# Optimization experiments

Measured on AMD Instinct MI355X. Metric: run time of the kernel, lower is better.

## Reference

```python
import jax, jax.numpy as jnp
import numpy as np

RESET_ALPHA = 0.9
THR_ALPHA = 0.95
DAMPENING = 0.3
REFRACTORY = 5


def setup_inputs() -> dict:
    key = jax.random.key(0)
    B, T, N = 16, 4096, 1024
    x = jax.random.normal(key, (B, T, N), dtype=jnp.float32)
    return {
        "x": x,
        "reset_gamma": jnp.ones((N,), jnp.float32),
        "thr_gamma": jnp.ones((N,), jnp.float32),
        "u0": jnp.zeros((N,), jnp.float32),
        "b0": jnp.zeros((N,), jnp.float32),
    }


def _spike(v):
    # SpikeFunction: heaviside forward, piecewise-quadratic surrogate gradient
    zf = (v > 0).astype(v.dtype)
    zb = jnp.where(v > 0, -0.5 * jnp.square(v - 1.0), 0.5 * jnp.square(v + 1.0))
    zb = jnp.where(jnp.abs(v) < 1.0, zb, 0.0) * DAMPENING
    # value == zf, gradient flows through zb (straight-through surrogate)
    return jax.lax.stop_gradient(zf - zb) + zb


def reference(x, reset_gamma, thr_gamma, u0, b0):
    B, T, N = x.shape
    al, bet = RESET_ALPHA, THR_ALPHA

    def step(carry, xt):
        u, b, q, last_z = carry  # all [B, N]
        u = al * u + (1.0 - al) * xt - last_z * reset_gamma
        z = _spike(u - b)
        z = jnp.where(q == 0, z, jnp.zeros_like(z))  # refractory mask
        q = jnp.maximum(0, q - 1)
        q = q + REFRACTORY * jax.lax.stop_gradient(z).astype(jnp.int32)
        b = bet * b + (1.0 - bet) * z * thr_gamma
        return (u, b, q, z), z

    u = jnp.broadcast_to(u0[None, :], (B, N)).astype(x.dtype)
    b = jnp.broadcast_to(b0[None, :], (B, N)).astype(x.dtype)
    q = jnp.zeros((B, N), jnp.int32)
    last_z = jnp.zeros((B, N), x.dtype)

    x_tbn = jnp.swapaxes(x, 0, 1)  # [T, B, N] for scan over time
    _, zs = jax.lax.scan(step, (u, b, q, last_z), x_tbn)
    return jnp.swapaxes(zs, 0, 1)  # [B, T, N]
```

## Files before the change

kernel.cpp:

```cpp
#include <hip/hip_runtime.h>


#pragma STDC FP_CONTRACT OFF

constexpr int B_LEN = 16;
constexpr int T_LEN = 4096;
constexpr int N_LEN = 1024;
constexpr int DEPTH = 16;
constexpr int NCH   = T_LEN / DEPTH;

__global__ __launch_bounds__(64)
void snn_fwd(const float* __restrict__ x,
             const float* __restrict__ rg_,
             const float* __restrict__ tg_,
             const float* __restrict__ u0_,
             const float* __restrict__ b0_,
             float* __restrict__ out)
{
    #pragma clang fp contract(off)
    const int id   = blockIdx.x * blockDim.x + threadIdx.x;
    const int b    = id >> 10;
    const int n    = id & 1023;
    const int loff = b * (T_LEN * N_LEN) + n;

    const float rg = rg_[n];
    const float tg = tg_[n];
    float u  = u0_[n];
    float bb = b0_[n];
    float lz = 0.0f;
    int allow = 0;

    float bufA[DEPTH], bufB[DEPTH];
    float zA[DEPTH],   zB[DEPTH];

#define LBURST(BUF, CIDX)                                                   \
    {                                                                       \
        const int cc_ = (CIDX) < NCH ? (CIDX) : (NCH - 1);                  \
        const float* p_ = x + (size_t)cc_ * (DEPTH * N_LEN) + loff;         \
        _Pragma("unroll")                                                   \
        for (int i_ = 0; i_ < DEPTH; ++i_) BUF[i_] = p_[(size_t)i_ * N_LEN];\
    }

#define SBURST(ZB_, CIDX)                                                   \
    {                                                                       \
        float* p_ = out + (size_t)(CIDX) * (DEPTH * N_LEN) + loff;          \
        _Pragma("unroll")                                                   \
        for (int i_ = 0; i_ < DEPTH; ++i_) p_[(size_t)i_ * N_LEN] = ZB_[i_];\
    }

#define COMPUTE(BUF, ZOUT, CIDX)                                            \
    {                                                                       \
        const int t0_ = (CIDX) * DEPTH;                                     \
        _Pragma("unroll")                                                   \
        for (int i_ = 0; i_ < DEPTH; ++i_) {                                \
            const float xt = BUF[i_];                                       \
            float m2 = 0.1f * xt;                                           \
            float s1 = __builtin_fmaf(0.9f, u, m2);                         \
            u = __builtin_fmaf(-lz, rg, s1);                                \
            const float v   = u - bb;                                       \
            const bool  pos = v > 0.0f;                                     \
            const float vm  = v + (pos ? -1.0f : 1.0f);                     \
            const float sq  = vm * vm;                                      \
            float zb = (pos ? -0.5f : 0.5f) * sq;                           \
            zb = (fabsf(v) < 1.0f) ? zb : 0.0f;                             \
            zb = zb * 0.3f;                                                 \
            const float zf = pos ? 1.0f : 0.0f;                             \
            const float d1 = zf - zb;                                       \
            float z = d1 + zb;                                              \
            z = ((t0_ + i_) >= allow) ? z : 0.0f;                           \
            allow = (z == 1.0f) ? (t0_ + i_ + 6) : allow;                   \
            float t1 = 0.05f * z;                                           \
            float t2 = t1 * tg;                                             \
            bb = __builtin_fmaf(0.95f, bb, t2);                             \
            lz = z;                                                         \
            ZOUT[i_] = z;                                                   \
        }                                                                   \
    }

    LBURST(bufA, 0)
    LBURST(bufB, 1)

    for (int k = 0; k < NCH; k += 2) {
        COMPUTE(bufA, zA, k)
        LBURST(bufA, k + 2)
        SBURST(zA, k)

        COMPUTE(bufB, zB, k + 1)
        LBURST(bufB, k + 3)
        SBURST(zB, k + 1)
    }
#undef LBURST
#undef SBURST
#undef COMPUTE
}

extern "C" void kernel_launch(void* const* d_in, const int* in_sizes, int n_in,
                              void* d_out, int out_size, void* d_ws, size_t ws_size,
                              hipStream_t stream)
{
    int xi = 0;
    for (int i = 1; i < n_in; ++i)
        if (in_sizes[i] > in_sizes[xi]) xi = i;

    const float* small[4];
    int k = 0;
    for (int i = 0; i < n_in && k < 4; ++i)
        if (i != xi) small[k++] = (const float*)d_in[i];

    const float* x  = (const float*)d_in[xi];
    float*      out = (float*)d_out;

    dim3 block(64);
    dim3 grid(B_LEN * N_LEN / 64);
    snn_fwd<<<grid, block, 0, stream>>>(x, small[0], small[1],
                                        small[2], small[3], out);
}
```

Baseline: 279.9 us.

## Use inline-asm loads with manual vmcnt waits and stream stores per step

Replaces the compiler-generated x loads with inline-asm global_load_dword instructions, followed by explicit s_waitcnt vmcnt fences with a sched_barrier. This keeps one 16-step chunk of loads in flight while the other chunk is computed, since the compiler may otherwise insert conservative full waits. Output spikes are now stored directly at each timestep instead of being staged in a register array and written in a burst, which frees registers. The wait counts assume stores also count toward vmcnt, so they are tied to the exact number and order of memory ops in the loop and are fragile if that changes.

Result: no change. 278.8 us (-0.4%).

```diff
diff --git a/kernel.cpp b/kernel.cpp
--- a/kernel.cpp
+++ b/kernel.cpp
@@ -9,7 +9,7 @@
 constexpr int DEPTH = 16;
 constexpr int NCH   = T_LEN / DEPTH;
 
-__global__ __launch_bounds__(64)
+__global__ __launch_bounds__(64, 1)
 void snn_fwd(const float* __restrict__ x,
              const float* __restrict__ rg_,
              const float* __restrict__ tg_,
@@ -18,10 +18,12 @@
              float* __restrict__ out)
 {
     #pragma clang fp contract(off)
-    const int id   = blockIdx.x * blockDim.x + threadIdx.x;
-    const int b    = id >> 10;
-    const int n    = id & 1023;
-    const int loff = b * (T_LEN * N_LEN) + n;
+    const int id = blockIdx.x * 64 + threadIdx.x;
+    const int b  = id >> 10;
+    const int n  = id & 1023;
+    const size_t loff = (size_t)b * (T_LEN * N_LEN) + n;
+    const float* xl = x + loff;
+    float*       ol = out + loff;
 
     const float rg = rg_[n];
     const float tg = tg_[n];
@@ -31,24 +33,29 @@
     int allow = 0;
 
     float bufA[DEPTH], bufB[DEPTH];
-    float zA[DEPTH],   zB[DEPTH];
 
 #define LBURST(BUF, CIDX)                                                   \
     {                                                                       \
         const int cc_ = (CIDX) < NCH ? (CIDX) : (NCH - 1);                  \
-        const float* p_ = x + (size_t)cc_ * (DEPTH * N_LEN) + loff;         \
+        const float* p_ = xl + (size_t)cc_ * (DEPTH * N_LEN);               \
         _Pragma("unroll")                                                   \
-        for (int i_ = 0; i_ < DEPTH; ++i_) BUF[i_] = p_[(size_t)i_ * N_LEN];\
+        for (int i_ = 0; i_ < DEPTH; ++i_) {                                \
+            const float* a_ = p_ + (size_t)i_ * N_LEN;                      \
+            asm volatile("global_load_dword %0, %1, off"                    \
+                         : "=v"(BUF[i_]) : "v"(a_) : "memory");             \
+        }                                                                   \
     }
 
-#define SBURST(ZB_, CIDX)                                                   \
-    {                                                                       \
-        float* p_ = out + (size_t)(CIDX) * (DEPTH * N_LEN) + loff;          \
-        _Pragma("unroll")                                                   \
-        for (int i_ = 0; i_ < DEPTH; ++i_) p_[(size_t)i_ * N_LEN] = ZB_[i_];\
-    }
+#define LWAIT(BUF, IMM)                                                     \
+    asm volatile("s_waitcnt vmcnt(" #IMM ")"                                \
+        : "+v"(BUF[0]),  "+v"(BUF[1]),  "+v"(BUF[2]),  "+v"(BUF[3]),        \
+          "+v"(BUF[4]),  "+v"(BUF[5]),  "+v"(BUF[6]),  "+v"(BUF[7]),        \
+          "+v"(BUF[8]),  "+v"(BUF[9]),  "+v"(BUF[10]), "+v"(BUF[11]),       \
+          "+v"(BUF[12]), "+v"(BUF[13]), "+v"(BUF[14]), "+v"(BUF[15])        \
+        :: "memory");                                                       \
+    __builtin_amdgcn_sched_barrier(0);
 
-#define COMPUTE(BUF, ZOUT, CIDX)                                            \
+#define COMPUTE(BUF, CIDX)                                                  \
     {                                                                       \
         const int t0_ = (CIDX) * DEPTH;                                     \
         _Pragma("unroll")                                                   \
@@ -73,24 +80,24 @@
             float t2 = t1 * tg;                                             \
             bb = __builtin_fmaf(0.95f, bb, t2);                             \
             lz = z;                                                         \
-            ZOUT[i_] = z;                                                   \
+            ol[(size_t)(t0_ + i_) * N_LEN] = z;                             \
         }                                                                   \
     }
 
     LBURST(bufA, 0)
     LBURST(bufB, 1)
+    LWAIT(bufA, 16)
 
     for (int k = 0; k < NCH; k += 2) {
-        COMPUTE(bufA, zA, k)
+        COMPUTE(bufA, k)
         LBURST(bufA, k + 2)
-        SBURST(zA, k)
-
-        COMPUTE(bufB, zB, k + 1)
+        LWAIT(bufB, 32)
+        COMPUTE(bufB, k + 1)
         LBURST(bufB, k + 3)
-        SBURST(zB, k + 1)
+        LWAIT(bufA, 32)
     }
 #undef LBURST
-#undef SBURST
+#undef LWAIT
 #undef COMPUTE
 }
 
```
